# Kernel optimization log

Hardware: AMD Instinct MI355X
Metric: run time of the kernel (lower is better)

The kernel has to match this reference:

```python
import jax, jax.numpy as jnp
from jax import lax
import numpy as np

EPSILON = 22.6  # Cech radius; ~mean pairwise distance of N(0,1) points in 256-d


def _betti1(x, eps):
    """Faithful port of compute_betti_number for one epsilon. x: (B,T,C)."""
    B, T, C = x.shape
    # pairwise squared distances; compare d2 < eps^2 == (dist < eps), avoids sqrt
    sq = jnp.sum(x * x, axis=-1)                                  # (B,T)
    d2 = sq[:, :, None] + sq[:, None, :] - 2.0 * jnp.einsum('btc,bsc->bts', x, x)
    adj = d2 < (eps * eps)                                        # (B,T,T) bool; diagonal True (dist 0 < eps), matching torch
    adj = lax.stop_gradient(adj)                                  # original detaches x before topology
    # original: n_edges = np.sum(adjacency) // 2, diagonal included
    n_edges = jnp.sum(adj, axis=(1, 2)).astype(jnp.int32) // 2    # (B,)
    # connected components via min-label propagation + pointer jumping
    labels0 = jnp.broadcast_to(jnp.arange(T, dtype=jnp.int32), (B, T))

    def cond(state):
        return state[1]

    def body(state):
        labels, _ = state
        # min label among neighbors (diag True includes self)
        prop = jnp.min(jnp.where(adj, labels[:, None, :], T), axis=2).astype(jnp.int32)
        new = jnp.minimum(labels, prop)
        new = jnp.take_along_axis(new, new, axis=1)               # pointer jump -> O(log) convergence
        return new, jnp.any(new != labels)

    labels, _ = lax.while_loop(cond, body, (labels0, jnp.array(True)))
    # converged label = min index in component -> count roots
    n_comp = jnp.sum(labels == jnp.arange(T, dtype=jnp.int32)[None, :], axis=1).astype(jnp.int32)
    betti1 = jnp.maximum(0, n_edges - T + n_comp)                 # max(0, E - V + C)
    return betti1


def reference(x_before, x_after):
    betti_before = _betti1(x_before, EPSILON)
    betti_after = _betti1(x_after, EPSILON)
    diff = betti_after.astype(jnp.float32) - betti_before.astype(jnp.float32)
    return jnp.mean(diff * diff)


def setup_inputs() -> dict:
    key = jax.random.key(0)
    k1, k2 = jax.random.split(key)
    B, T, C = 4, 4096, 256
    x_before = jax.random.normal(k1, (B, T, C), dtype=jnp.float32)
    x_after = jax.random.normal(k2, (B, T, C), dtype=jnp.float32)
    return {"x_before": x_before, "x_after": x_after}
```

## Files before the change

kernel.cpp:

```cpp
#include <hip/hip_runtime.h>
#include <stdint.h>

#define TDIM 4096
#define CDIM 256
#define NMAT 8

typedef __attribute__((ext_vector_type(8))) __bf16 bf16x8;
typedef __attribute__((ext_vector_type(4))) float f32x4;

__device__ __forceinline__ unsigned short f2bf(float f) {
  unsigned int u = __float_as_uint(f);
  return (unsigned short)((u + 0x7FFFu + ((u >> 16) & 1u)) >> 16);
}
__device__ __forceinline__ void g2lds16(const void* g, void* l) {
  __builtin_amdgcn_global_load_lds((__attribute__((address_space(1))) void*)(void*)g,
                                   (__attribute__((address_space(3))) void*)l, 16, 0, 0);
}
__device__ __forceinline__ unsigned long long shfl_xor_u64(unsigned long long v, int m) {
  int lo = __shfl_xor((int)(unsigned int)(v & 0xFFFFFFFFull), m);
  int hi = __shfl_xor((int)(unsigned int)(v >> 32), m);
  return ((unsigned long long)(unsigned int)hi << 32) | (unsigned int)lo;
}

__global__ __launch_bounds__(256) void prep_kernel(
    const float* __restrict__ xb, const float* __restrict__ xa,
    unsigned short* __restrict__ xhi, float* __restrict__ sq) {
  const int wid = threadIdx.x >> 6, lane = threadIdx.x & 63;
  const int gr = blockIdx.x * 4 + wid;
  const int mb = gr >> 12;
  const size_t rowoff = (size_t)gr * CDIM;
  const float* src = (mb < 4) ? (xb + rowoff) : (xa + rowoff - (size_t)4 * TDIM * CDIM);

  float4 v = ((const float4*)src)[lane];
  float vv[4] = {v.x, v.y, v.z, v.w};
  unsigned short h[4];
  float ss = 0.f;
#pragma unroll
  for (int c = 0; c < 4; ++c) {
    h[c] = f2bf(vv[c]);
    ss += vv[c] * vv[c];
  }
  *(ushort4*)&xhi[rowoff + lane * 4] = make_ushort4(h[0], h[1], h[2], h[3]);
#pragma unroll
  for (int off = 32; off; off >>= 1) ss += __shfl_down(ss, off);
  if (lane == 0) sq[gr] = ss;
}

__global__ __launch_bounds__(256) void prep4_kernel(
    const float* __restrict__ src0, unsigned short* __restrict__ xhi,
    float* __restrict__ sq4) {
  const int wid = threadIdx.x >> 6, lane = threadIdx.x & 63;
  const int gr = blockIdx.x * 4 + wid;
  const size_t rowoff = (size_t)gr * CDIM;
  float4 v = ((const float4*)(src0 + rowoff))[lane];
  float vv[4] = {v.x, v.y, v.z, v.w};
  unsigned short h[4];
  float ss = 0.f;
#pragma unroll
  for (int c = 0; c < 4; ++c) {
    h[c] = f2bf(vv[c]);
    ss += vv[c] * vv[c];
  }
  *(ushort4*)&xhi[rowoff + lane * 4] = make_ushort4(h[0], h[1], h[2], h[3]);
#pragma unroll
  for (int off = 32; off; off >>= 1) ss += __shfl_down(ss, off);
  if (lane == 0) sq4[gr] = ss;
}

__global__ __launch_bounds__(256) void gram_kernel(
    const unsigned short* __restrict__ xhi, const float* __restrict__ sq,
    unsigned long long* __restrict__ adj, int mb_base, int mbits) {
  __shared__ unsigned short As[128 * 64];
  __shared__ unsigned short Bs[128 * 64];

  const int tid = threadIdx.x;
  const int wid = tid >> 6, lane = tid & 63;
  const int wr = wid >> 1, wc = wid & 1;

  const int mbl = blockIdx.x & ((1 << mbits) - 1);
  const int mb = mb_base + mbl;
  int rem = blockIdx.x >> mbits;
  int ti = 0;
  while (rem >= 32 - ti) { rem -= 32 - ti; ++ti; }
  const int tj = ti + rem;

  const unsigned short* hi = xhi + (size_t)mbl * TDIM * CDIM;
  const float* sqm = sq + (size_t)mb * TDIM;

  f32x4 acc[4][4] = {};

  const int ldrow = (lane >> 3);
  const int ldcol = ((lane & 7) ^ ldrow) * 8;

  for (int ks = 0; ks < 4; ++ks) {
    const int kcol = ks * 64;
    __syncthreads();
#pragma unroll
    for (int i = 0; i < 4; ++i) {
      const int chunk = wid * 4 + i;
      const int row = chunk * 8 + ldrow;
      g2lds16(hi + (size_t)(ti * 128 + row) * CDIM + kcol + ldcol, &As[chunk * 512]);
      g2lds16(hi + (size_t)(tj * 128 + row) * CDIM + kcol + ldcol, &Bs[chunk * 512]);
    }
    asm volatile("s_waitcnt vmcnt(0)" ::: "memory");
    __syncthreads();
#pragma unroll
    for (int kk = 0; kk < 2; ++kk) {
      bf16x8 a[4], b[4];
      const int hi16 = lane >> 4;
#pragma unroll
      for (int m = 0; m < 4; ++m) {
        const int row = wr * 64 + m * 16 + (lane & 15);
        a[m] = *(const bf16x8*)&As[row * 64 + (((kk * 4 + hi16) ^ (row & 7)) * 8)];
      }
#pragma unroll
      for (int n = 0; n < 4; ++n) {
        const int row = wc * 64 + n * 16 + (lane & 15);
        b[n] = *(const bf16x8*)&Bs[row * 64 + (((kk * 4 + hi16) ^ (row & 7)) * 8)];
      }
#pragma unroll
      for (int m = 0; m < 4; ++m)
#pragma unroll
        for (int n = 0; n < 4; ++n)
          acc[m][n] = __builtin_amdgcn_mfma_f32_16x16x32_bf16(a[m], b[n], acc[m][n], 0, 0, 0);
    }
  }

  const float EPS2 = (float)(22.6 * 22.6);
  unsigned long long* adjm = adj + (size_t)mb * TDIM * 64;
  const int gt = (lane >> 2) & 3;
  const int mtgt = lane >> 4, rtgt = lane & 3;
  unsigned long long vrow = 0;

  float4 srv[4];
#pragma unroll
  for (int m = 0; m < 4; ++m)
    srv[m] = *(const float4*)&sqm[ti * 128 + wr * 64 + m * 16 + (lane >> 4) * 4];
  float scv[4];
#pragma unroll
  for (int n = 0; n < 4; ++n) scv[n] = sqm[tj * 128 + wc * 64 + n * 16 + (lane & 15)];

#pragma unroll
  for (int m = 0; m < 4; ++m) {
#pragma unroll
    for (int r = 0; r < 4; ++r) {
      const float srr = ((const float*)&srv[m])[r];
      unsigned long long bl[4];
#pragma unroll
      for (int n = 0; n < 4; ++n) {
        const float d2 = srr + scv[n] - 2.0f * acc[m][n][r];
        bl[n] = __ballot(d2 < EPS2);
      }
      if (m == mtgt && r == rtgt)
        vrow = ((bl[0] >> (16 * gt)) & 0xFFFFULL)         | (((bl[1] >> (16 * gt)) & 0xFFFFULL) << 16) |
               (((bl[2] >> (16 * gt)) & 0xFFFFULL) << 32) | (((bl[3] >> (16 * gt)) & 0xFFFFULL) << 48);
    }
  }
  adjm[(size_t)(ti * 128 + wr * 64 + lane) * 64 + tj * 2 + wc] = vrow;

  if (ti != tj) {
    const unsigned long long mk[6] = {
        0x5555555555555555ull, 0x3333333333333333ull, 0x0F0F0F0F0F0F0F0Full,
        0x00FF00FF00FF00FFull, 0x0000FFFF0000FFFFull, 0x00000000FFFFFFFFull};
#pragma unroll
    for (int s = 0; s < 6; ++s) {
      const int d = 1 << s;
      const unsigned long long m = mk[s];
      unsigned long long t = shfl_xor_u64(vrow, d);
      if ((lane & d) == 0) vrow = (vrow & m) | ((t & m) << d);
      else                 vrow = (vrow & ~m) | ((t & ~m) >> d);
    }
    adjm[(size_t)(tj * 128 + wc * 64 + lane) * 64 + ti * 2 + wr] = vrow;
  }
}

__global__ __launch_bounds__(256) void cc_pass1_kernel(const unsigned long long* __restrict__ adj,
                                                       int* __restrict__ gnxt,
                                                       unsigned int* __restrict__ edgepart) {
  __shared__ unsigned int wcnt[4];
  const int wid = threadIdx.x >> 6, lane = threadIdx.x & 63;
  const int grow = blockIdx.x * 4 + wid;
  unsigned long long w = adj[(size_t)grow * 64 + lane];
  int cand = w ? (lane * 64 + __ffsll(w) - 1) : 0x7fffffff;
  unsigned int c = (unsigned int)__popcll(w);
#pragma unroll
  for (int off = 32; off; off >>= 1) {
    cand = min(cand, __shfl_down(cand, off));
    c += __shfl_down(c, off);
  }
  if (lane == 0) {
    gnxt[grow] = min(cand, grow & (TDIM - 1));
    wcnt[wid] = c;
  }
  __syncthreads();
  if (threadIdx.x == 0)
    edgepart[blockIdx.x] = wcnt[0] + wcnt[1] + wcnt[2] + wcnt[3];
}

__global__ __launch_bounds__(1024) void cc_iter_kernel(const unsigned long long* __restrict__ adj,
                                                       const int* __restrict__ gnxt,
                                                       int* __restrict__ ncomp) {
  __shared__ int lab[TDIM];
  __shared__ int nxt[TDIM];
  __shared__ int changed;
  __shared__ int croots;
  const int mb = blockIdx.x;
  const unsigned long long* A = adj + (size_t)mb * TDIM * 64;
  const int tid = threadIdx.x;

  for (int i = tid; i < TDIM; i += 1024) nxt[i] = gnxt[mb * TDIM + i];
  __syncthreads();
  for (int i = tid; i < TDIM; i += 1024) lab[i] = nxt[nxt[i]];
  __syncthreads();

  for (int it = 0; it < 96; ++it) {
    if (tid == 0) changed = 0;
    __syncthreads();
    for (int i = tid; i < TDIM; i += 1024) {
      const int cur = lab[i];
      int mn = cur;
      if (cur > 0) {
        for (int wd = 0; wd < 64 && mn > 0; ++wd) {
          unsigned long long w = A[(size_t)i * 64 + wd];
          while (w && mn > 0) {
            const int bit = __ffsll(w) - 1;
            w &= w - 1;
            mn = min(mn, lab[wd * 64 + bit]);
          }
        }
        if (mn < cur) changed = 1;
      }
      nxt[i] = mn;
    }
    __syncthreads();
    const int ch = changed;
    for (int i = tid; i < TDIM; i += 1024) lab[i] = nxt[nxt[i]];
    __syncthreads();
    if (!ch) break;
  }

  if (tid == 0) croots = 0;
  __syncthreads();
  int c = 0;
  for (int i = tid; i < TDIM; i += 1024) c += (lab[i] == i);
  atomicAdd(&croots, c);
  __syncthreads();
  if (tid == 0) ncomp[mb] = croots;
}

__global__ __launch_bounds__(512) void final_kernel(const unsigned int* __restrict__ edgepart,
                                                    const int* __restrict__ ncomp,
                                                    float* __restrict__ out) {
  __shared__ unsigned long long es[8];
  const int wid = threadIdx.x >> 6, lane = threadIdx.x & 63;
  unsigned long long s = 0;
  for (int i = lane; i < 1024; i += 64) s += edgepart[wid * 1024 + i];
#pragma unroll
  for (int off = 32; off; off >>= 1) s += __shfl_down(s, off);
  if (lane == 0) es[wid] = s;
  __syncthreads();
  if (threadIdx.x == 0) {
    double acc = 0.0;
    for (int b = 0; b < 4; ++b) {
      long long e0 = (long long)(es[b] >> 1);
      long long bet0 = e0 - TDIM + (long long)ncomp[b];
      if (bet0 < 0) bet0 = 0;
      long long e1 = (long long)(es[4 + b] >> 1);
      long long bet1 = e1 - TDIM + (long long)ncomp[4 + b];
      if (bet1 < 0) bet1 = 0;
      double d = (double)(bet1 - bet0);
      acc += d * d;
    }
    out[0] = (float)(acc * 0.25);
  }
}

extern "C" void kernel_launch(void* const* d_in, const int* in_sizes, int n_in,
                              void* d_out, int out_size, void* d_ws, size_t ws_size,
                              hipStream_t stream) {
  (void)in_sizes; (void)n_in; (void)out_size;
  const float* xb = (const float*)d_in[0];
  const float* xa = (const float*)d_in[1];
  char* ws = (char*)d_ws;

  const bool big = (ws_size == 0) || (ws_size >= ((size_t)34 << 20));

  if (big) {
    const size_t XHI_OFF = 0;
    const size_t ADJ_OFF = (size_t)NMAT * TDIM * CDIM * 2;
    const size_t SQ_OFF  = ADJ_OFF + (size_t)NMAT * TDIM * 64 * 8;
    const size_t NC_OFF  = SQ_OFF + (size_t)NMAT * TDIM * 4;
    const size_t GNXT_OFF = NC_OFF + 64;
    const size_t EDGE_OFF = GNXT_OFF + (size_t)NMAT * TDIM * 4;

    unsigned short* xhi = (unsigned short*)(ws + XHI_OFF);
    unsigned long long* adj = (unsigned long long*)(ws + ADJ_OFF);
    float* sq = (float*)(ws + SQ_OFF);
    int* ncomp = (int*)(ws + NC_OFF);
    int* gnxt = (int*)(ws + GNXT_OFF);
    unsigned int* edgepart = (unsigned int*)(ws + EDGE_OFF);

    prep_kernel<<<NMAT * TDIM / 4, 256, 0, stream>>>(xb, xa, xhi, sq);
    gram_kernel<<<NMAT * 528, 256, 0, stream>>>(xhi, sq, adj, 0, 3);
    cc_pass1_kernel<<<NMAT * TDIM / 4, 256, 0, stream>>>(adj, gnxt, edgepart);
    cc_iter_kernel<<<NMAT, 1024, 0, stream>>>(adj, gnxt, ncomp);
    final_kernel<<<1, 512, 0, stream>>>(edgepart, ncomp, (float*)d_out);
  } else {
    const size_t XHI_OFF = 0;
    const size_t ADJ_OFF = (size_t)4 * TDIM * CDIM * 2;
    const size_t SQ_OFF  = ADJ_OFF + (size_t)NMAT * TDIM * 64 * 8;
    const size_t NC_OFF  = SQ_OFF + (size_t)NMAT * TDIM * 4;
    const size_t GNXT_OFF = NC_OFF + 64;
    const size_t EDGE_OFF = GNXT_OFF + (size_t)NMAT * TDIM * 4;

    unsigned short* xhi = (unsigned short*)(ws + XHI_OFF);
    unsigned long long* adj = (unsigned long long*)(ws + ADJ_OFF);
    float* sq = (float*)(ws + SQ_OFF);
    int* ncomp = (int*)(ws + NC_OFF);
    int* gnxt = (int*)(ws + GNXT_OFF);
    unsigned int* edgepart = (unsigned int*)(ws + EDGE_OFF);

    prep4_kernel<<<TDIM, 256, 0, stream>>>(xb, xhi, sq);
    gram_kernel<<<4 * 528, 256, 0, stream>>>(xhi, sq, adj, 0, 2);
    prep4_kernel<<<TDIM, 256, 0, stream>>>(xa, xhi, sq + (size_t)4 * TDIM);
    gram_kernel<<<4 * 528, 256, 0, stream>>>(xhi, sq, adj, 4, 2);
    cc_pass1_kernel<<<NMAT * TDIM / 4, 256, 0, stream>>>(adj, gnxt, edgepart);
    cc_iter_kernel<<<NMAT, 1024, 0, stream>>>(adj, gnxt, ncomp);
    final_kernel<<<1, 512, 0, stream>>>(edgepart, ncomp, (float*)d_out);
  }
}
```

Baseline: 86.21 us.

## Double-buffer LDS tiles in gram kernel and hoist norm loads

The gram kernel now keeps two LDS buffers for the A and B tiles. Global-to-LDS loads for the next K slice are issued before the MFMAs on the current slice, so load latency overlaps with compute. A partial vmcnt wait and raw s_barrier calls replace the full drain plus __syncthreads. The squared-norm loads move before the main loop so their latency also hides behind compute. The cost is doubled LDS per block (64KB), which may lower occupancy, and the loop relies on in-order vmcnt accounting being correct.

Measured after the change: 92.05 us. +6.8%, slower.

```diff
diff --git a/kernel.cpp b/kernel.cpp
--- a/kernel.cpp
+++ b/kernel.cpp
@@ -70,8 +70,8 @@
 __global__ __launch_bounds__(256) void gram_kernel(
     const unsigned short* __restrict__ xhi, const float* __restrict__ sq,
     unsigned long long* __restrict__ adj, int mb_base, int mbits) {
-  __shared__ unsigned short As[128 * 64];
-  __shared__ unsigned short Bs[128 * 64];
+  __shared__ unsigned short As[2][128 * 64];
+  __shared__ unsigned short Bs[2][128 * 64];
 
   const int tid = threadIdx.x;
   const int wid = tid >> 6, lane = tid & 63;
@@ -87,23 +87,45 @@
   const unsigned short* hi = xhi + (size_t)mbl * TDIM * CDIM;
   const float* sqm = sq + (size_t)mb * TDIM;
 
+  float4 srv[4];
+#pragma unroll
+  for (int m = 0; m < 4; ++m)
+    srv[m] = *(const float4*)&sqm[ti * 128 + wr * 64 + m * 16 + (lane >> 4) * 4];
+  float scv[4];
+#pragma unroll
+  for (int n = 0; n < 4; ++n) scv[n] = sqm[tj * 128 + wc * 64 + n * 16 + (lane & 15)];
+
   f32x4 acc[4][4] = {};
 
   const int ldrow = (lane >> 3);
   const int ldcol = ((lane & 7) ^ ldrow) * 8;
 
+#define STAGE(KS, BUF)                                                              \
+  {                                                                                 \
+    const int kcol = (KS) * 64;                                                     \
+    _Pragma("unroll") for (int i = 0; i < 4; ++i) {                                 \
+      const int chunk = wid * 4 + i;                                                \
+      const int row = chunk * 8 + ldrow;                                            \
+      g2lds16(hi + (size_t)(ti * 128 + row) * CDIM + kcol + ldcol,                  \
+              &As[BUF][chunk * 512]);                                               \
+      g2lds16(hi + (size_t)(tj * 128 + row) * CDIM + kcol + ldcol,                  \
+              &Bs[BUF][chunk * 512]);                                               \
+    }                                                                               \
+  }
+
+  STAGE(0, 0);
+
+#pragma unroll
   for (int ks = 0; ks < 4; ++ks) {
-    const int kcol = ks * 64;
-    __syncthreads();
-#pragma unroll
-    for (int i = 0; i < 4; ++i) {
-      const int chunk = wid * 4 + i;
-      const int row = chunk * 8 + ldrow;
-      g2lds16(hi + (size_t)(ti * 128 + row) * CDIM + kcol + ldcol, &As[chunk * 512]);
-      g2lds16(hi + (size_t)(tj * 128 + row) * CDIM + kcol + ldcol, &Bs[chunk * 512]);
-    }
-    asm volatile("s_waitcnt vmcnt(0)" ::: "memory");
-    __syncthreads();
+    const int cur = ks & 1;
+    if (ks < 3) {
+      STAGE(ks + 1, cur ^ 1);
+      asm volatile("s_waitcnt vmcnt(8)" ::: "memory");
+    } else {
+      asm volatile("s_waitcnt vmcnt(0)" ::: "memory");
+    }
+    __builtin_amdgcn_s_barrier();
+    asm volatile("" ::: "memory");
 #pragma unroll
     for (int kk = 0; kk < 2; ++kk) {
       bf16x8 a[4], b[4];
@@ -111,12 +133,12 @@
 #pragma unroll
       for (int m = 0; m < 4; ++m) {
         const int row = wr * 64 + m * 16 + (lane & 15);
-        a[m] = *(const bf16x8*)&As[row * 64 + (((kk * 4 + hi16) ^ (row & 7)) * 8)];
+        a[m] = *(const bf16x8*)&As[cur][row * 64 + (((kk * 4 + hi16) ^ (row & 7)) * 8)];
       }
 #pragma unroll
       for (int n = 0; n < 4; ++n) {
         const int row = wc * 64 + n * 16 + (lane & 15);
-        b[n] = *(const bf16x8*)&Bs[row * 64 + (((kk * 4 + hi16) ^ (row & 7)) * 8)];
+        b[n] = *(const bf16x8*)&Bs[cur][row * 64 + (((kk * 4 + hi16) ^ (row & 7)) * 8)];
       }
 #pragma unroll
       for (int m = 0; m < 4; ++m)
@@ -124,21 +146,19 @@
         for (int n = 0; n < 4; ++n)
           acc[m][n] = __builtin_amdgcn_mfma_f32_16x16x32_bf16(a[m], b[n], acc[m][n], 0, 0, 0);
     }
-  }
+    if (ks < 3) {
+      asm volatile("" ::: "memory");
+      __builtin_amdgcn_s_barrier();
+      asm volatile("" ::: "memory");
+    }
+  }
+#undef STAGE
 
   const float EPS2 = (float)(22.6 * 22.6);
   unsigned long long* adjm = adj + (size_t)mb * TDIM * 64;
   const int gt = (lane >> 2) & 3;
   const int mtgt = lane >> 4, rtgt = lane & 3;
   unsigned long long vrow = 0;
-
-  float4 srv[4];
-#pragma unroll
-  for (int m = 0; m < 4; ++m)
-    srv[m] = *(const float4*)&sqm[ti * 128 + wr * 64 + m * 16 + (lane >> 4) * 4];
-  float scv[4];
-#pragma unroll
-  for (int n = 0; n < 4; ++n) scv[n] = sqm[tj * 128 + wc * 64 + n * 16 + (lane & 15)];
 
 #pragma unroll
   for (int m = 0; m < 4; ++m) {
```
